# Kernel optimization log

Measured on AMD Instinct MI355X. Metric: run time of the kernel, lower is better.

## Reference

```python
import jax, jax.numpy as jnp
import numpy as np

N_CLASSES = 256
GT_CLASSES = 21
DIM = 384
EPS = 1e-12  # matches torch F.normalize default eps


def setup_inputs() -> dict:
    key = jax.random.key(0)
    k1, k2, k3 = jax.random.split(key, 3)
    features = jax.random.normal(k1, (4, 256, 256, DIM), dtype=jnp.float32)
    weight = jax.random.uniform(k2, (4, 256, 256), dtype=jnp.float32)
    cluster_centers = jax.random.normal(k3, (N_CLASSES, DIM), dtype=jnp.float32)
    pseudo_assignment = (jnp.arange(N_CLASSES) % GT_CLASSES).astype(jnp.int32)
    return {
        "features": features,
        "weight": weight,
        "cluster_centers": cluster_centers,
        "pseudo_assignment": pseudo_assignment,
    }


def _l2norm(x, axis):
    # torch F.normalize: x / max(||x||, eps)
    n = jnp.sqrt(jnp.sum(x * x, axis=axis, keepdims=True))
    return x / jnp.maximum(n, EPS)


def reference(features, weight, cluster_centers, pseudo_assignment):
    lead_shape = features.shape[:-1]
    feats = features.reshape(-1, features.shape[-1])        # [N, D]
    w = weight.reshape(-1)                                   # [N]

    normed_clusters = _l2norm(cluster_centers, axis=1)       # [K, D]
    normed_features = _l2norm(feats, axis=1)                 # [N, D]

    inner_products = normed_features @ normed_clusters.T     # [N, K]
    class_labels = jnp.argmax(inner_products, axis=1)        # [N]

    # -(one_hot(labels) * inner_products).sum(1) == -inner_products[n, labels[n]]
    cluster_loss = -jnp.take_along_axis(
        inner_products, class_labels[:, None], axis=1
    )[:, 0]                                                  # [N]

    loss = jnp.mean(cluster_loss * w)

    pseudo_segs_pred = class_labels.reshape(lead_shape)
    segs_pred = pseudo_assignment[pseudo_segs_pred].astype(jnp.int64)
    return pseudo_segs_pred, segs_pred, loss
```

## Files before the change

### kernel.cpp

```cpp
#include <hip/hip_runtime.h>
#include <hip/hip_bf16.h>

#define NTOT (4*256*256)
#define DIM 384
#define KCL 256
#define BM 64
#define TBS 256
#define GRID_MAIN (NTOT/BM)
#define NT 12
#define EPS 1e-12f

#define AB(p) ((p) * 8192)
#define SMEM_BYTES 16384

typedef __attribute__((ext_vector_type(8))) _Float16 f16x8;
typedef __attribute__((ext_vector_type(4))) float f32x4;

__global__ void prep_clusters(const float* __restrict__ cc,
                              _Float16* __restrict__ bh,
                              _Float16* __restrict__ bl) {
    int j = blockIdx.x, l = threadIdx.x;
    float v[6]; float ssq = 0.f;
#pragma unroll
    for (int i = 0; i < 6; ++i) { v[i] = cc[j*DIM + l + 64*i]; ssq = fmaf(v[i], v[i], ssq); }
#pragma unroll
    for (int off = 32; off >= 1; off >>= 1) ssq += __shfl_xor(ssq, off);
    float inv = 1.f / fmaxf(sqrtf(ssq), EPS);
    const int w = j >> 6, n = (j >> 4) & 3, nl = j & 15;
#pragma unroll
    for (int i = 0; i < 6; ++i) {
        int d = l + 64 * i;
        float x = v[i] * inv;
        _Float16 h  = (_Float16)x;
        _Float16 lo = (_Float16)(x - (float)h);
        size_t idx = (size_t)((((((d >> 5)*4 + w)*4 + n)*4 + ((d >> 3) & 3))*16 + nl)*8
                              + (d & 7));
        bh[idx] = h;
        bl[idx] = lo;
    }
}

__global__ __launch_bounds__(TBS, 3)
void kmeans_main(const float* __restrict__ A,
                 const float* __restrict__ W,
                 const _Float16* __restrict__ Bh,
                 const _Float16* __restrict__ Bl,
                 const int*   __restrict__ PA,
                 float* __restrict__ out,
                 float* __restrict__ partial)
{
    __shared__ unsigned char smem[SMEM_BYTES];

    const int tid  = threadIdx.x;
    const int wv   = tid >> 6;
    const int lane = tid & 63;
    const int g    = lane >> 4;
    const int l15  = lane & 15;
    const int sw   = (l15 >> 1) & 3;
    const int row0 = blockIdx.x * BM;
    const int arow = tid >> 2, achk = tid & 3;
    const int awb  = (((arow << 2) + (achk ^ ((arow >> 1) & 3))) << 4);
    const int fa   = l15 * 64 + ((g ^ sw) << 4);

    const float* ap = A + (size_t)(row0 + arow) * DIM + achk * 8;
    const unsigned char* bsh = (const unsigned char*)Bh + (size_t)(wv * 4) * 1024 + lane * 16;
    const unsigned char* bsl = (const unsigned char*)Bl + (size_t)(wv * 4) * 1024 + lane * 16;

    f32x4 acc[4][4];
#pragma unroll
    for (int m = 0; m < 4; ++m)
#pragma unroll
        for (int n = 0; n < 4; ++n) acc[m][n] = (f32x4){0.f, 0.f, 0.f, 0.f};
    float ssq = 0.f;

    f16x8  bfh[4], bfl[4];
    float4 sA[2][2];

    auto LDA = [&](int s, int tt) {
        sA[s][0] = *(const float4*)(ap + tt * 32);
        sA[s][1] = *(const float4*)(ap + tt * 32 + 4);
    };
    auto LDBH = [&](int tt) {
#pragma unroll
        for (int n = 0; n < 4; ++n)
            bfh[n] = *(const f16x8*)(bsh + (size_t)(tt * 16 + n) * 1024);
    };
    auto LDBL = [&](int tt) {
#pragma unroll
        for (int n = 0; n < 4; ++n)
            bfl[n] = *(const f16x8*)(bsl + (size_t)(tt * 16 + n) * 1024);
    };
    auto CVTW = [&](int s, int p) {
        float av[8] = {sA[s][0].x, sA[s][0].y, sA[s][0].z, sA[s][0].w,
                       sA[s][1].x, sA[s][1].y, sA[s][1].z, sA[s][1].w};
        f16x8 h8, l8;
#pragma unroll
        for (int e = 0; e < 8; ++e) {
            _Float16 hh = (_Float16)av[e];
            h8[e] = hh;
            l8[e] = (_Float16)(av[e] - (float)hh);
            ssq = fmaf(av[e], av[e], ssq);
        }
        *(f16x8*)(smem + AB(p) + awb) = h8;
        *(f16x8*)(smem + AB(p) + 4096 + awb) = l8;
    };

    LDA(0, 0);
    LDBL(0); LDBH(0);
    LDA(1, 1);
    CVTW(0, 0);
    asm volatile("s_waitcnt lgkmcnt(0)" ::: "memory");
    __builtin_amdgcn_s_barrier();

#pragma unroll
    for (int t = 0; t < NT; ++t) {
        if (t + 2 < NT) LDA((t + 2) & 1, t + 2);

        f16x8 ahf[4], alf[4];
#pragma unroll
        for (int m = 0; m < 4; ++m) {
            ahf[m] = *(const f16x8*)(smem + AB(t & 1) + fa + m * 1024);
            alf[m] = *(const f16x8*)(smem + AB(t & 1) + 4096 + fa + m * 1024);
        }
        if (t + 1 < NT) CVTW((t + 1) & 1, (t + 1) & 1);

        __builtin_amdgcn_s_setprio(1);
#pragma unroll
        for (int m = 0; m < 4; ++m)
#pragma unroll
            for (int n = 0; n < 4; ++n)
                acc[m][n] = __builtin_amdgcn_mfma_f32_16x16x32_f16(ahf[m], bfh[n], acc[m][n], 0, 0, 0);
#pragma unroll
        for (int m = 0; m < 4; ++m)
#pragma unroll
            for (int n = 0; n < 4; ++n)
                acc[m][n] = __builtin_amdgcn_mfma_f32_16x16x32_f16(ahf[m], bfl[n], acc[m][n], 0, 0, 0);
        __builtin_amdgcn_s_setprio(0);
        if (t + 1 < NT) LDBL(t + 1);
        __builtin_amdgcn_s_setprio(1);
#pragma unroll
        for (int m = 0; m < 4; ++m)
#pragma unroll
            for (int n = 0; n < 4; ++n)
                acc[m][n] = __builtin_amdgcn_mfma_f32_16x16x32_f16(alf[m], bfh[n], acc[m][n], 0, 0, 0);
        __builtin_amdgcn_s_setprio(0);
        if (t + 1 < NT) LDBH(t + 1);

        asm volatile("s_waitcnt lgkmcnt(0)" ::: "memory");
        __builtin_amdgcn_s_barrier();
    }
    __syncthreads();

    float* rowssq = (float*)smem;
    float* wvalp  = (float*)(smem + 256);
    int*   wcolp  = (int*)(smem + 1280);

    ssq += __shfl_xor(ssq, 1);
    ssq += __shfl_xor(ssq, 2);
    if (achk == 0) rowssq[arow] = ssq;

#pragma unroll
    for (int m = 0; m < 4; ++m) {
#pragma unroll
        for (int j = 0; j < 4; ++j) {
            float best = acc[m][0][j];
            int   bc   = 64*wv + l15;
#pragma unroll
            for (int n = 1; n < 4; ++n) {
                float v = acc[m][n][j];
                int   c = 64*wv + 16*n + l15;
                if (v > best) { best = v; bc = c; }
            }
#pragma unroll
            for (int off = 1; off < 16; off <<= 1) {
                float ov = __shfl_xor(best, off);
                int   oc = __shfl_xor(bc, off);
                if (ov > best || (ov == best && oc < bc)) { best = ov; bc = oc; }
            }
            if (l15 == 0) {
                wvalp[wv * BM + 16*m + 4*g + j] = best;
                wcolp[wv * BM + 16*m + 4*g + j] = bc;
            }
        }
    }
    __syncthreads();

    if (tid < BM) {
        int r = tid;
        float best = wvalp[r]; int bc = wcolp[r];
#pragma unroll
        for (int w = 1; w < 4; ++w) {
            float ov = wvalp[w * BM + r]; int oc = wcolp[w * BM + r];
            if (ov > best || (ov == best && oc < bc)) { best = ov; bc = oc; }
        }
        float inv = 1.f / fmaxf(sqrtf(rowssq[r]), EPS);
        int gr = row0 + r;
        out[gr]        = (float)bc;
        out[NTOT + gr] = (float)PA[bc];
        float lsum = -(best * inv) * W[gr];
#pragma unroll
        for (int off = 32; off >= 1; off >>= 1) lsum += __shfl_xor(lsum, off);
        if (tid == 0) partial[blockIdx.x] = lsum;
    }
}

__global__ void loss_reduce(const float* __restrict__ partial, float* __restrict__ out_loss) {
    __shared__ float s[256];
    float v = 0.f;
    for (int i = threadIdx.x; i < GRID_MAIN; i += 256) v += partial[i];
    s[threadIdx.x] = v;
    __syncthreads();
    for (int off = 128; off >= 1; off >>= 1) {
        if ((int)threadIdx.x < off) s[threadIdx.x] += s[threadIdx.x + off];
        __syncthreads();
    }
    if (threadIdx.x == 0) out_loss[0] = s[0] * (1.0f / (float)NTOT);
}

extern "C" void kernel_launch(void* const* d_in, const int* in_sizes, int n_in,
                              void* d_out, int out_size, void* d_ws, size_t ws_size,
                              hipStream_t stream) {
    const float* features = (const float*)d_in[0];
    const float* weight   = (const float*)d_in[1];
    const float* cc       = (const float*)d_in[2];
    const int*   pa       = (const int*)d_in[3];
    float* out = (float*)d_out;

    _Float16* bh   = (_Float16*)d_ws;
    _Float16* bl   = bh + KCL * DIM;
    float* partial = (float*)(bl + KCL * DIM);

    hipLaunchKernelGGL(prep_clusters, dim3(KCL), dim3(64), 0, stream, cc, bh, bl);
    hipLaunchKernelGGL(kmeans_main, dim3(GRID_MAIN), dim3(TBS), 0, stream,
                       features, weight, bh, bl, pa, out, partial);
    hipLaunchKernelGGL(loss_reduce, dim3(1), dim3(256), 0, stream, partial, out + 2 * NTOT);
}
```

Measured before the change: 194.9 us.

## Stage two K-tiles per barrier to halve block synchronizations

```diff
diff --git a/kernel.cpp b/kernel.cpp
--- a/kernel.cpp
+++ b/kernel.cpp
@@ -7,11 +7,11 @@
 #define BM 64
 #define TBS 256
 #define GRID_MAIN (NTOT/BM)
-#define NT 12
+#define NSTEP 6
 #define EPS 1e-12f
 
-#define AB(p) ((p) * 8192)
-#define SMEM_BYTES 16384
+#define AB(p) ((p) * 16384)
+#define SMEM_BYTES 32768
 
 typedef __attribute__((ext_vector_type(8))) _Float16 f16x8;
 typedef __attribute__((ext_vector_type(4))) float f32x4;
@@ -74,11 +74,13 @@
     float ssq = 0.f;
 
     f16x8  bfh[4], bfl[4];
-    float4 sA[2][2];
-
-    auto LDA = [&](int s, int tt) {
-        sA[s][0] = *(const float4*)(ap + tt * 32);
-        sA[s][1] = *(const float4*)(ap + tt * 32 + 4);
+    float4 sA[4];
+
+    auto LDA = [&](int T) {
+        sA[0] = *(const float4*)(ap + T * 64);
+        sA[1] = *(const float4*)(ap + T * 64 + 4);
+        sA[2] = *(const float4*)(ap + T * 64 + 32);
+        sA[3] = *(const float4*)(ap + T * 64 + 36);
     };
     auto LDBH = [&](int tt) {
 #pragma unroll
@@ -90,40 +92,33 @@
         for (int n = 0; n < 4; ++n)
             bfl[n] = *(const f16x8*)(bsl + (size_t)(tt * 16 + n) * 1024);
     };
-    auto CVTW = [&](int s, int p) {
-        float av[8] = {sA[s][0].x, sA[s][0].y, sA[s][0].z, sA[s][0].w,
-                       sA[s][1].x, sA[s][1].y, sA[s][1].z, sA[s][1].w};
-        f16x8 h8, l8;
-#pragma unroll
-        for (int e = 0; e < 8; ++e) {
-            _Float16 hh = (_Float16)av[e];
-            h8[e] = hh;
-            l8[e] = (_Float16)(av[e] - (float)hh);
-            ssq = fmaf(av[e], av[e], ssq);
-        }
-        *(f16x8*)(smem + AB(p) + awb) = h8;
-        *(f16x8*)(smem + AB(p) + 4096 + awb) = l8;
-    };
-
-    LDA(0, 0);
-    LDBL(0); LDBH(0);
-    LDA(1, 1);
-    CVTW(0, 0);
-    asm volatile("s_waitcnt lgkmcnt(0)" ::: "memory");
-    __builtin_amdgcn_s_barrier();
-
-#pragma unroll
-    for (int t = 0; t < NT; ++t) {
-        if (t + 2 < NT) LDA((t + 2) & 1, t + 2);
-
-        f16x8 ahf[4], alf[4];
+    auto CVTW = [&](int p) {
+#pragma unroll
+        for (int h = 0; h < 2; ++h) {
+            float av[8] = {sA[2*h].x, sA[2*h].y, sA[2*h].z, sA[2*h].w,
+                           sA[2*h+1].x, sA[2*h+1].y, sA[2*h+1].z, sA[2*h+1].w};
+            f16x8 h8, l8;
+#pragma unroll
+            for (int e = 0; e < 8; ++e) {
+                _Float16 hh = (_Float16)av[e];
+                h8[e] = hh;
+                l8[e] = (_Float16)(av[e] - (float)hh);
+                ssq = fmaf(av[e], av[e], ssq);
+            }
+            *(f16x8*)(smem + AB(p) + h * 8192 + awb) = h8;
+            *(f16x8*)(smem + AB(p) + h * 8192 + 4096 + awb) = l8;
+        }
+    };
+
+    f16x8 ahf[4], alf[4];
+    auto READA = [&](int p, int kh) {
 #pragma unroll
         for (int m = 0; m < 4; ++m) {
-            ahf[m] = *(const f16x8*)(smem + AB(t & 1) + fa + m * 1024);
-            alf[m] = *(const f16x8*)(smem + AB(t & 1) + 4096 + fa + m * 1024);
-        }
-        if (t + 1 < NT) CVTW((t + 1) & 1, (t + 1) & 1);
-
+            ahf[m] = *(const f16x8*)(smem + AB(p) + kh * 8192 + fa + m * 1024);
+            alf[m] = *(const f16x8*)(smem + AB(p) + kh * 8192 + 4096 + fa + m * 1024);
+        }
+    };
+    auto MFMA3 = [&](int nextTile, bool doLoad) {
         __builtin_amdgcn_s_setprio(1);
 #pragma unroll
         for (int m = 0; m < 4; ++m)
@@ -136,7 +131,7 @@
             for (int n = 0; n < 4; ++n)
                 acc[m][n] = __builtin_amdgcn_mfma_f32_16x16x32_f16(ahf[m], bfl[n], acc[m][n], 0, 0, 0);
         __builtin_amdgcn_s_setprio(0);
-        if (t + 1 < NT) LDBL(t + 1);
+        if (doLoad) LDBL(nextTile);
         __builtin_amdgcn_s_setprio(1);
 #pragma unroll
         for (int m = 0; m < 4; ++m)
@@ -144,10 +139,29 @@
             for (int n = 0; n < 4; ++n)
                 acc[m][n] = __builtin_amdgcn_mfma_f32_16x16x32_f16(alf[m], bfh[n], acc[m][n], 0, 0, 0);
         __builtin_amdgcn_s_setprio(0);
-        if (t + 1 < NT) LDBH(t + 1);
+        if (doLoad) LDBH(nextTile);
+    };
+
+    LDA(0);
+    LDBL(0); LDBH(0);
+    CVTW(0);
+    asm volatile("s_waitcnt lgkmcnt(0)" ::: "memory");
+    __builtin_amdgcn_s_barrier();
+
+#pragma unroll
+    for (int t = 0; t < NSTEP; ++t) {
+        if (t + 1 < NSTEP) LDA(t + 1);
+
+        READA(t & 1, 0);
+        MFMA3(2 * t + 1, true);
+
+        READA(t & 1, 1);
+        if (t + 1 < NSTEP) CVTW((t + 1) & 1);
 
         asm volatile("s_waitcnt lgkmcnt(0)" ::: "memory");
         __builtin_amdgcn_s_barrier();
+
+        MFMA3(2 * t + 2, t + 1 < NSTEP);
     }
     __syncthreads();
 
```

After: 191.4 us. About the same (-1.8%).

## Use single fp16 GEMM with fp32 rescue pass for near-tie rows

Applied to the files above, without the earlier changes.

```diff
diff --git a/kernel.cpp b/kernel.cpp
--- a/kernel.cpp
+++ b/kernel.cpp
@@ -9,16 +9,18 @@
 #define GRID_MAIN (NTOT/BM)
 #define NT 12
 #define EPS 1e-12f
-
-#define AB(p) ((p) * 8192)
-#define SMEM_BYTES 16384
+#define DELTA 1e-3f
+#define RBLK 512
+#define WPB (GRID_MAIN/RBLK)
+
+#define SMEM_BYTES 8192
 
 typedef __attribute__((ext_vector_type(8))) _Float16 f16x8;
 typedef __attribute__((ext_vector_type(4))) float f32x4;
 
 __global__ void prep_clusters(const float* __restrict__ cc,
                               _Float16* __restrict__ bh,
-                              _Float16* __restrict__ bl) {
+                              float* __restrict__ invn) {
     int j = blockIdx.x, l = threadIdx.x;
     float v[6]; float ssq = 0.f;
 #pragma unroll
@@ -26,17 +28,14 @@
 #pragma unroll
     for (int off = 32; off >= 1; off >>= 1) ssq += __shfl_xor(ssq, off);
     float inv = 1.f / fmaxf(sqrtf(ssq), EPS);
+    if (l == 0) invn[j] = inv;
     const int w = j >> 6, n = (j >> 4) & 3, nl = j & 15;
 #pragma unroll
     for (int i = 0; i < 6; ++i) {
         int d = l + 64 * i;
-        float x = v[i] * inv;
-        _Float16 h  = (_Float16)x;
-        _Float16 lo = (_Float16)(x - (float)h);
         size_t idx = (size_t)((((((d >> 5)*4 + w)*4 + n)*4 + ((d >> 3) & 3))*16 + nl)*8
                               + (d & 7));
-        bh[idx] = h;
-        bl[idx] = lo;
+        bh[idx] = (_Float16)(v[i] * inv);
     }
 }
 
@@ -44,10 +43,10 @@
 void kmeans_main(const float* __restrict__ A,
                  const float* __restrict__ W,
                  const _Float16* __restrict__ Bh,
-                 const _Float16* __restrict__ Bl,
                  const int*   __restrict__ PA,
                  float* __restrict__ out,
-                 float* __restrict__ partial)
+                 float* __restrict__ partial,
+                 unsigned long long* __restrict__ flags)
 {
     __shared__ unsigned char smem[SMEM_BYTES];
 
@@ -64,7 +63,6 @@
 
     const float* ap = A + (size_t)(row0 + arow) * DIM + achk * 8;
     const unsigned char* bsh = (const unsigned char*)Bh + (size_t)(wv * 4) * 1024 + lane * 16;
-    const unsigned char* bsl = (const unsigned char*)Bl + (size_t)(wv * 4) * 1024 + lane * 16;
 
     f32x4 acc[4][4];
 #pragma unroll
@@ -73,7 +71,7 @@
         for (int n = 0; n < 4; ++n) acc[m][n] = (f32x4){0.f, 0.f, 0.f, 0.f};
     float ssq = 0.f;
 
-    f16x8  bfh[4], bfl[4];
+    f16x8  bfh[4];
     float4 sA[2][2];
 
     auto LDA = [&](int s, int tt) {
@@ -85,28 +83,20 @@
         for (int n = 0; n < 4; ++n)
             bfh[n] = *(const f16x8*)(bsh + (size_t)(tt * 16 + n) * 1024);
     };
-    auto LDBL = [&](int tt) {
-#pragma unroll
-        for (int n = 0; n < 4; ++n)
-            bfl[n] = *(const f16x8*)(bsl + (size_t)(tt * 16 + n) * 1024);
-    };
     auto CVTW = [&](int s, int p) {
         float av[8] = {sA[s][0].x, sA[s][0].y, sA[s][0].z, sA[s][0].w,
                        sA[s][1].x, sA[s][1].y, sA[s][1].z, sA[s][1].w};
-        f16x8 h8, l8;
+        f16x8 h8;
 #pragma unroll
         for (int e = 0; e < 8; ++e) {
-            _Float16 hh = (_Float16)av[e];
-            h8[e] = hh;
-            l8[e] = (_Float16)(av[e] - (float)hh);
+            h8[e] = (_Float16)av[e];
             ssq = fmaf(av[e], av[e], ssq);
         }
-        *(f16x8*)(smem + AB(p) + awb) = h8;
-        *(f16x8*)(smem + AB(p) + 4096 + awb) = l8;
+        *(f16x8*)(smem + p * 4096 + awb) = h8;
     };
 
     LDA(0, 0);
-    LDBL(0); LDBH(0);
+    LDBH(0);
     LDA(1, 1);
     CVTW(0, 0);
     asm volatile("s_waitcnt lgkmcnt(0)" ::: "memory");
@@ -116,13 +106,13 @@
     for (int t = 0; t < NT; ++t) {
         if (t + 2 < NT) LDA((t + 2) & 1, t + 2);
 
-        f16x8 ahf[4], alf[4];
-#pragma unroll
-        for (int m = 0; m < 4; ++m) {
-            ahf[m] = *(const f16x8*)(smem + AB(t & 1) + fa + m * 1024);
-            alf[m] = *(const f16x8*)(smem + AB(t & 1) + 4096 + fa + m * 1024);
-        }
+        f16x8 ahf[4];
+#pragma unroll
+        for (int m = 0; m < 4; ++m)
+            ahf[m] = *(const f16x8*)(smem + (t & 1) * 4096 + fa + m * 1024);
         if (t + 1 < NT) CVTW((t + 1) & 1, (t + 1) & 1);
+        asm volatile("s_waitcnt lgkmcnt(0)" ::: "memory");
+        __builtin_amdgcn_s_barrier();
 
         __builtin_amdgcn_s_setprio(1);
 #pragma unroll
@@ -130,30 +120,15 @@
 #pragma unroll
             for (int n = 0; n < 4; ++n)
                 acc[m][n] = __builtin_amdgcn_mfma_f32_16x16x32_f16(ahf[m], bfh[n], acc[m][n], 0, 0, 0);
-#pragma unroll
-        for (int m = 0; m < 4; ++m)
-#pragma unroll
-            for (int n = 0; n < 4; ++n)
-                acc[m][n] = __builtin_amdgcn_mfma_f32_16x16x32_f16(ahf[m], bfl[n], acc[m][n], 0, 0, 0);
-        __builtin_amdgcn_s_setprio(0);
-        if (t + 1 < NT) LDBL(t + 1);
-        __builtin_amdgcn_s_setprio(1);
-#pragma unroll
-        for (int m = 0; m < 4; ++m)
-#pragma unroll
-            for (int n = 0; n < 4; ++n)
-                acc[m][n] = __builtin_amdgcn_mfma_f32_16x16x32_f16(alf[m], bfh[n], acc[m][n], 0, 0, 0);
         __builtin_amdgcn_s_setprio(0);
         if (t + 1 < NT) LDBH(t + 1);
-
-        asm volatile("s_waitcnt lgkmcnt(0)" ::: "memory");
-        __builtin_amdgcn_s_barrier();
     }
     __syncthreads();
 
     float* rowssq = (float*)smem;
     float* wvalp  = (float*)(smem + 256);
-    int*   wcolp  = (int*)(smem + 1280);
+    float* wsecp  = (float*)(smem + 1280);
+    int*   wcolp  = (int*)(smem + 2304);
 
     ssq += __shfl_xor(ssq, 1);
     ssq += __shfl_xor(ssq, 2);
@@ -163,23 +138,23 @@
     for (int m = 0; m < 4; ++m) {
 #pragma unroll
         for (int j = 0; j < 4; ++j) {
-            float best = acc[m][0][j];
-            int   bc   = 64*wv + l15;
+            float b0 = acc[m][0][j]; int i0 = 64*wv + l15; float s0 = -3.0e38f;
 #pragma unroll
             for (int n = 1; n < 4; ++n) {
-                float v = acc[m][n][j];
-                int   c = 64*wv + 16*n + l15;
-                if (v > best) { best = v; bc = c; }
+                float v = acc[m][n][j]; int c = 64*wv + 16*n + l15;
+                if (v > b0) { s0 = b0; b0 = v; i0 = c; } else { s0 = fmaxf(s0, v); }
             }
 #pragma unroll
             for (int off = 1; off < 16; off <<= 1) {
-                float ov = __shfl_xor(best, off);
-                int   oc = __shfl_xor(bc, off);
-                if (ov > best || (ov == best && oc < bc)) { best = ov; bc = oc; }
+                float ov = __shfl_xor(b0, off);
+                int   oi = __shfl_xor(i0, off);
+                float os = __shfl_xor(s0, off);
+                if (ov > b0 || (ov == b0 && oi < i0)) { s0 = fmaxf(os, b0); b0 = ov; i0 = oi; }
+                else                                  { s0 = fmaxf(s0, ov); }
             }
             if (l15 == 0) {
-                wvalp[wv * BM + 16*m + 4*g + j] = best;
-                wcolp[wv * BM + 16*m + 4*g + j] = bc;
+                int r = 16*m + 4*g + j;
+                wvalp[wv * BM + r] = b0; wsecp[wv * BM + r] = s0; wcolp[wv * BM + r] = i0;
             }
         }
     }
@@ -187,34 +162,145 @@
 
     if (tid < BM) {
         int r = tid;
-        float best = wvalp[r]; int bc = wcolp[r];
+        float b = wvalp[r], s = wsecp[r]; int i = wcolp[r];
 #pragma unroll
         for (int w = 1; w < 4; ++w) {
-            float ov = wvalp[w * BM + r]; int oc = wcolp[w * BM + r];
-            if (ov > best || (ov == best && oc < bc)) { best = ov; bc = oc; }
+            float bw = wvalp[w * BM + r], sw2 = wsecp[w * BM + r]; int iw = wcolp[w * BM + r];
+            if (bw > b || (bw == b && iw < i)) { s = fmaxf(b, sw2); b = bw; i = iw; }
+            else                               { s = fmaxf(s, bw); }
         }
         float inv = 1.f / fmaxf(sqrtf(rowssq[r]), EPS);
         int gr = row0 + r;
-        out[gr]        = (float)bc;
-        out[NTOT + gr] = (float)PA[bc];
-        float lsum = -(best * inv) * W[gr];
+        out[gr]        = (float)i;
+        out[NTOT + gr] = (float)PA[i];
+        bool amb = (b - s) < DELTA;
+        unsigned long long mask = __ballot(amb);
+        float lsum = amb ? 0.f : -(b * inv) * W[gr];
 #pragma unroll
         for (int off = 32; off >= 1; off >>= 1) lsum += __shfl_xor(lsum, off);
-        if (tid == 0) partial[blockIdx.x] = lsum;
-    }
-}
-
-__global__ void loss_reduce(const float* __restrict__ partial, float* __restrict__ out_loss) {
+        if (tid == 0) { partial[blockIdx.x] = lsum; flags[blockIdx.x] = mask; }
+    }
+}
+
+__global__ __launch_bounds__(256)
+void rescue(const float* __restrict__ A, const float* __restrict__ W,
+            const float* __restrict__ cc, const float* __restrict__ invn,
+            const unsigned long long* __restrict__ flags,
+            const int* __restrict__ PA,
+            float* __restrict__ out, float* __restrict__ partial2)
+{
+    __shared__ float rows[4][8][DIM];
+    __shared__ int   rlist[64 * WPB];
+    __shared__ int   rcount;
+    __shared__ float wsum[4];
+    const int tid = threadIdx.x, wv = tid >> 6, lane = tid & 63;
+    const int b = blockIdx.x;
+
+    if (tid == 0) {
+        int c = 0;
+#pragma unroll
+        for (int w = 0; w < WPB; ++w) {
+            unsigned long long m = flags[b * WPB + w];
+            while (m) {
+                int bit = __ffsll((long long)m) - 1;
+                m &= m - 1;
+                rlist[c++] = (b * WPB + w) * 64 + bit;
+            }
+        }
+        rcount = c;
+    }
+    __syncthreads();
+    const int nb = rcount;
+    const float in0 = invn[lane], in1 = invn[64 + lane],
+                in2 = invn[128 + lane], in3 = invn[192 + lane];
+    float lacc = 0.f;
+    const int nbatch = (nb + 31) >> 5;
+
+    for (int bt = 0; bt < nbatch; ++bt) {
+        const int base = bt * 32 + wv * 8;
+        int rIdx[8]; float ssq8[8];
+#pragma unroll
+        for (int i = 0; i < 8; ++i) {
+            int li = base + i;
+            int r = rlist[li < nb ? li : 0];
+            rIdx[i] = r;
+            float ps = 0.f;
+#pragma unroll
+            for (int c = 0; c < 6; ++c) {
+                float x = A[(size_t)r * DIM + c*64 + lane];
+                rows[wv][i][c*64 + lane] = x;
+                ps = fmaf(x, x, ps);
+            }
+#pragma unroll
+            for (int off = 32; off >= 1; off >>= 1) ps += __shfl_xor(ps, off);
+            ssq8[i] = ps;
+        }
+        __syncthreads();
+        float d0[8], d1[8], d2[8], d3[8];
+#pragma unroll
+        for (int i = 0; i < 8; ++i) { d0[i]=0.f; d1[i]=0.f; d2[i]=0.f; d3[i]=0.f; }
+#pragma unroll 4
+        for (int k = 0; k < DIM; k += 4) {
+            float4 rv[8];
+#pragma unroll
+            for (int i = 0; i < 8; ++i) rv[i] = *(const float4*)&rows[wv][i][k];
+            float4 c0 = *(const float4*)&cc[(size_t)(0*64 + lane)*DIM + k];
+            float4 c1 = *(const float4*)&cc[(size_t)(1*64 + lane)*DIM + k];
+            float4 c2 = *(const float4*)&cc[(size_t)(2*64 + lane)*DIM + k];
+            float4 c3 = *(const float4*)&cc[(size_t)(3*64 + lane)*DIM + k];
+#pragma unroll
+            for (int i = 0; i < 8; ++i) {
+                d0[i] = fmaf(c0.x,rv[i].x, fmaf(c0.y,rv[i].y, fmaf(c0.z,rv[i].z, fmaf(c0.w,rv[i].w, d0[i]))));
+                d1[i] = fmaf(c1.x,rv[i].x, fmaf(c1.y,rv[i].y, fmaf(c1.z,rv[i].z, fmaf(c1.w,rv[i].w, d1[i]))));
+                d2[i] = fmaf(c2.x,rv[i].x, fmaf(c2.y,rv[i].y, fmaf(c2.z,rv[i].z, fmaf(c2.w,rv[i].w, d2[i]))));
+                d3[i] = fmaf(c3.x,rv[i].x, fmaf(c3.y,rv[i].y, fmaf(c3.z,rv[i].z, fmaf(c3.w,rv[i].w, d3[i]))));
+            }
+        }
+#pragma unroll
+        for (int i = 0; i < 8; ++i) {
+            if (base + i < nb) {
+                float v0 = d0[i]*in0, v1 = d1[i]*in1, v2 = d2[i]*in2, v3 = d3[i]*in3;
+                float best = v0; int bj = lane;
+                { if (v1 > best) { best = v1; bj = 64 + lane; } }
+                { if (v2 > best) { best = v2; bj = 128 + lane; } }
+                { if (v3 > best) { best = v3; bj = 192 + lane; } }
+#pragma unroll
+                for (int off = 1; off < 64; off <<= 1) {
+                    float ov = __shfl_xor(best, off);
+                    int   oj = __shfl_xor(bj, off);
+                    if (ov > best || (ov == best && oj < bj)) { best = ov; bj = oj; }
+                }
+                if (lane == 0) {
+                    int r = rIdx[i];
+                    float inva = 1.f / fmaxf(sqrtf(ssq8[i]), EPS);
+                    out[r]        = (float)bj;
+                    out[NTOT + r] = (float)PA[bj];
+                    lacc = fmaf(-(best * inva), W[r], lacc);
+                }
+            }
+        }
+        __syncthreads();
+    }
+    if (lane == 0) wsum[wv] = lacc;
+    __syncthreads();
+    if (tid == 0) partial2[b] = ((wsum[0] + wsum[1]) + (wsum[2] + wsum[3]));
+}
+
+__global__ void loss_reduce(const float* __restrict__ partial,
+                            const float* __restrict__ partial2,
+                            float* __restrict__ out_loss) {
     __shared__ float s[256];
+    const int t = threadIdx.x;
     float v = 0.f;
-    for (int i = threadIdx.x; i < GRID_MAIN; i += 256) v += partial[i];
-    s[threadIdx.x] = v;
+    for (int i = t; i < GRID_MAIN; i += 256) v += partial[i];
+    for (int i = t; i < RBLK; i += 256) v += partial2[i];
+    s[t] = v;
     __syncthreads();
     for (int off = 128; off >= 1; off >>= 1) {
-        if ((int)threadIdx.x < off) s[threadIdx.x] += s[threadIdx.x + off];
+        if (t < off) s[t] += s[t + off];
         __syncthreads();
     }
-    if (threadIdx.x == 0) out_loss[0] = s[0] * (1.0f / (float)NTOT);
+    if (t == 0) out_loss[0] = s[0] * (1.0f / (float)NTOT);
 }
 
 extern "C" void kernel_launch(void* const* d_in, const int* in_sizes, int n_in,
@@ -226,12 +312,17 @@
     const int*   pa       = (const int*)d_in[3];
     float* out = (float*)d_out;
 
-    _Float16* bh   = (_Float16*)d_ws;
-    _Float16* bl   = bh + KCL * DIM;
-    float* partial = (float*)(bl + KCL * DIM);
-
-    hipLaunchKernelGGL(prep_clusters, dim3(KCL), dim3(64), 0, stream, cc, bh, bl);
+    _Float16* bh = (_Float16*)d_ws;
+    unsigned long long* flags = (unsigned long long*)(bh + KCL * DIM);
+    float* invn    = (float*)(flags + GRID_MAIN);
+    float* partial = invn + KCL;
+    float* partial2 = partial + GRID_MAIN;
+
+    hipLaunchKernelGGL(prep_clusters, dim3(KCL), dim3(64), 0, stream, cc, bh, invn);
     hipLaunchKernelGGL(kmeans_main, dim3(GRID_MAIN), dim3(TBS), 0, stream,
-                       features, weight, bh, bl, pa, out, partial);
-    hipLaunchKernelGGL(loss_reduce, dim3(1), dim3(256), 0, stream, partial, out + 2 * NTOT);
-}
+                       features, weight, bh, pa, out, partial, flags);
+    hipLaunchKernelGGL(rescue, dim3(RBLK), dim3(256), 0, stream,
+                       features, weight, cc, invn, flags, pa, out, partial2);
+    hipLaunchKernelGGL(loss_reduce, dim3(1), dim3(256), 0, stream,
+                       partial, partial2, out + 2 * NTOT);
+}
```

After: 283.4 us. +45.4%, slower.

## Use single fp16 MFMA pass with fp32 rescoring of ambiguous rows

Applied to the files above, without the earlier changes.

```diff
diff --git a/kernel.cpp b/kernel.cpp
--- a/kernel.cpp
+++ b/kernel.cpp
@@ -9,16 +9,17 @@
 #define GRID_MAIN (NTOT/BM)
 #define NT 12
 #define EPS 1e-12f
-
-#define AB(p) ((p) * 8192)
-#define SMEM_BYTES 16384
+#define DELTA 0.09f
+#define CAP 12
+
+#define SMEM_BYTES 8192
 
 typedef __attribute__((ext_vector_type(8))) _Float16 f16x8;
 typedef __attribute__((ext_vector_type(4))) float f32x4;
 
 __global__ void prep_clusters(const float* __restrict__ cc,
                               _Float16* __restrict__ bh,
-                              _Float16* __restrict__ bl) {
+                              float* __restrict__ invn) {
     int j = blockIdx.x, l = threadIdx.x;
     float v[6]; float ssq = 0.f;
 #pragma unroll
@@ -26,25 +27,23 @@
 #pragma unroll
     for (int off = 32; off >= 1; off >>= 1) ssq += __shfl_xor(ssq, off);
     float inv = 1.f / fmaxf(sqrtf(ssq), EPS);
+    if (l == 0) invn[j] = inv;
     const int w = j >> 6, n = (j >> 4) & 3, nl = j & 15;
 #pragma unroll
     for (int i = 0; i < 6; ++i) {
         int d = l + 64 * i;
-        float x = v[i] * inv;
-        _Float16 h  = (_Float16)x;
-        _Float16 lo = (_Float16)(x - (float)h);
         size_t idx = (size_t)((((((d >> 5)*4 + w)*4 + n)*4 + ((d >> 3) & 3))*16 + nl)*8
                               + (d & 7));
-        bh[idx] = h;
-        bl[idx] = lo;
-    }
-}
-
-__global__ __launch_bounds__(TBS, 3)
+        bh[idx] = (_Float16)(v[i] * inv);
+    }
+}
+
+__global__ __launch_bounds__(TBS, 4)
 void kmeans_main(const float* __restrict__ A,
                  const float* __restrict__ W,
                  const _Float16* __restrict__ Bh,
-                 const _Float16* __restrict__ Bl,
+                 const float* __restrict__ cc,
+                 const float* __restrict__ invn,
                  const int*   __restrict__ PA,
                  float* __restrict__ out,
                  float* __restrict__ partial)
@@ -64,7 +63,6 @@
 
     const float* ap = A + (size_t)(row0 + arow) * DIM + achk * 8;
     const unsigned char* bsh = (const unsigned char*)Bh + (size_t)(wv * 4) * 1024 + lane * 16;
-    const unsigned char* bsl = (const unsigned char*)Bl + (size_t)(wv * 4) * 1024 + lane * 16;
 
     f32x4 acc[4][4];
 #pragma unroll
@@ -73,7 +71,7 @@
         for (int n = 0; n < 4; ++n) acc[m][n] = (f32x4){0.f, 0.f, 0.f, 0.f};
     float ssq = 0.f;
 
-    f16x8  bfh[4], bfl[4];
+    f16x8  bfh[4];
     float4 sA[2][2];
 
     auto LDA = [&](int s, int tt) {
@@ -85,28 +83,20 @@
         for (int n = 0; n < 4; ++n)
             bfh[n] = *(const f16x8*)(bsh + (size_t)(tt * 16 + n) * 1024);
     };
-    auto LDBL = [&](int tt) {
-#pragma unroll
-        for (int n = 0; n < 4; ++n)
-            bfl[n] = *(const f16x8*)(bsl + (size_t)(tt * 16 + n) * 1024);
-    };
     auto CVTW = [&](int s, int p) {
         float av[8] = {sA[s][0].x, sA[s][0].y, sA[s][0].z, sA[s][0].w,
                        sA[s][1].x, sA[s][1].y, sA[s][1].z, sA[s][1].w};
-        f16x8 h8, l8;
+        f16x8 h8;
 #pragma unroll
         for (int e = 0; e < 8; ++e) {
-            _Float16 hh = (_Float16)av[e];
-            h8[e] = hh;
-            l8[e] = (_Float16)(av[e] - (float)hh);
+            h8[e] = (_Float16)av[e];
             ssq = fmaf(av[e], av[e], ssq);
         }
-        *(f16x8*)(smem + AB(p) + awb) = h8;
-        *(f16x8*)(smem + AB(p) + 4096 + awb) = l8;
+        *(f16x8*)(smem + p * 4096 + awb) = h8;
     };
 
     LDA(0, 0);
-    LDBL(0); LDBH(0);
+    LDBH(0);
     LDA(1, 1);
     CVTW(0, 0);
     asm volatile("s_waitcnt lgkmcnt(0)" ::: "memory");
@@ -116,13 +106,13 @@
     for (int t = 0; t < NT; ++t) {
         if (t + 2 < NT) LDA((t + 2) & 1, t + 2);
 
-        f16x8 ahf[4], alf[4];
-#pragma unroll
-        for (int m = 0; m < 4; ++m) {
-            ahf[m] = *(const f16x8*)(smem + AB(t & 1) + fa + m * 1024);
-            alf[m] = *(const f16x8*)(smem + AB(t & 1) + 4096 + fa + m * 1024);
-        }
+        f16x8 ahf[4];
+#pragma unroll
+        for (int m = 0; m < 4; ++m)
+            ahf[m] = *(const f16x8*)(smem + (t & 1) * 4096 + fa + m * 1024);
         if (t + 1 < NT) CVTW((t + 1) & 1, (t + 1) & 1);
+        asm volatile("s_waitcnt lgkmcnt(0)" ::: "memory");
+        __builtin_amdgcn_s_barrier();
 
         __builtin_amdgcn_s_setprio(1);
 #pragma unroll
@@ -130,30 +120,23 @@
 #pragma unroll
             for (int n = 0; n < 4; ++n)
                 acc[m][n] = __builtin_amdgcn_mfma_f32_16x16x32_f16(ahf[m], bfh[n], acc[m][n], 0, 0, 0);
-#pragma unroll
-        for (int m = 0; m < 4; ++m)
-#pragma unroll
-            for (int n = 0; n < 4; ++n)
-                acc[m][n] = __builtin_amdgcn_mfma_f32_16x16x32_f16(ahf[m], bfl[n], acc[m][n], 0, 0, 0);
-        __builtin_amdgcn_s_setprio(0);
-        if (t + 1 < NT) LDBL(t + 1);
-        __builtin_amdgcn_s_setprio(1);
-#pragma unroll
-        for (int m = 0; m < 4; ++m)
-#pragma unroll
-            for (int n = 0; n < 4; ++n)
-                acc[m][n] = __builtin_amdgcn_mfma_f32_16x16x32_f16(alf[m], bfh[n], acc[m][n], 0, 0, 0);
         __builtin_amdgcn_s_setprio(0);
         if (t + 1 < NT) LDBH(t + 1);
-
-        asm volatile("s_waitcnt lgkmcnt(0)" ::: "memory");
-        __builtin_amdgcn_s_barrier();
-    }
-    __syncthreads();
-
-    float* rowssq = (float*)smem;
+    }
+    __syncthreads();
+
+    float* rowssq = (float*)(smem);
     float* wvalp  = (float*)(smem + 256);
-    int*   wcolp  = (int*)(smem + 1280);
+    float* wsecp  = (float*)(smem + 1280);
+    int*   wcolp  = (int*)(smem + 2304);
+    float* rowtop = (float*)(smem + 3328);
+    float* rowinv = (float*)(smem + 3584);
+    float* lrowS  = (float*)(smem + 3840);
+    unsigned long long* fmaskS = (unsigned long long*)(smem + 4096);
+    int*   ccount = (int*)(smem + 4160);
+    int*   clist  = (int*)(smem + 4416);
+    float* wrv    = (float*)(smem + 7488);
+    int*   wrc    = (int*)(smem + 7552);
 
     ssq += __shfl_xor(ssq, 1);
     ssq += __shfl_xor(ssq, 2);
@@ -163,23 +146,23 @@
     for (int m = 0; m < 4; ++m) {
 #pragma unroll
         for (int j = 0; j < 4; ++j) {
-            float best = acc[m][0][j];
-            int   bc   = 64*wv + l15;
+            float b0 = acc[m][0][j]; int i0 = 64*wv + l15; float s0 = -3.0e38f;
 #pragma unroll
             for (int n = 1; n < 4; ++n) {
-                float v = acc[m][n][j];
-                int   c = 64*wv + 16*n + l15;
-                if (v > best) { best = v; bc = c; }
+                float v = acc[m][n][j]; int c = 64*wv + 16*n + l15;
+                if (v > b0) { s0 = b0; b0 = v; i0 = c; } else { s0 = fmaxf(s0, v); }
             }
 #pragma unroll
             for (int off = 1; off < 16; off <<= 1) {
-                float ov = __shfl_xor(best, off);
-                int   oc = __shfl_xor(bc, off);
-                if (ov > best || (ov == best && oc < bc)) { best = ov; bc = oc; }
+                float ov = __shfl_xor(b0, off);
+                int   oi = __shfl_xor(i0, off);
+                float os = __shfl_xor(s0, off);
+                if (ov > b0 || (ov == b0 && oi < i0)) { s0 = fmaxf(os, b0); b0 = ov; i0 = oi; }
+                else                                  { s0 = fmaxf(s0, ov); }
             }
             if (l15 == 0) {
-                wvalp[wv * BM + 16*m + 4*g + j] = best;
-                wcolp[wv * BM + 16*m + 4*g + j] = bc;
+                int r = 16*m + 4*g + j;
+                wvalp[wv * BM + r] = b0; wsecp[wv * BM + r] = s0; wcolp[wv * BM + r] = i0;
             }
         }
     }
@@ -187,20 +170,94 @@
 
     if (tid < BM) {
         int r = tid;
-        float best = wvalp[r]; int bc = wcolp[r];
+        if (r < 64) ccount[r] = 0;
+        float b = wvalp[r], s = wsecp[r]; int i = wcolp[r];
 #pragma unroll
         for (int w = 1; w < 4; ++w) {
-            float ov = wvalp[w * BM + r]; int oc = wcolp[w * BM + r];
-            if (ov > best || (ov == best && oc < bc)) { best = ov; bc = oc; }
+            float bw = wvalp[w * BM + r], sw2 = wsecp[w * BM + r]; int iw = wcolp[w * BM + r];
+            if (bw > b || (bw == b && iw < i)) { s = fmaxf(b, sw2); b = bw; i = iw; }
+            else                               { s = fmaxf(s, bw); }
         }
         float inv = 1.f / fmaxf(sqrtf(rowssq[r]), EPS);
+        rowtop[r] = b; rowinv[r] = inv;
+        bool amb = (b - s) < DELTA;
+        unsigned long long msk = __ballot(amb);
         int gr = row0 + r;
-        out[gr]        = (float)bc;
-        out[NTOT + gr] = (float)PA[bc];
-        float lsum = -(best * inv) * W[gr];
-#pragma unroll
-        for (int off = 32; off >= 1; off >>= 1) lsum += __shfl_xor(lsum, off);
-        if (tid == 0) partial[blockIdx.x] = lsum;
+        if (!amb) {
+            out[gr]        = (float)i;
+            out[NTOT + gr] = (float)PA[i];
+        }
+        lrowS[r] = amb ? 0.f : -(b * inv) * W[gr];
+        if (tid == 0) fmaskS[0] = msk;
+    }
+    __syncthreads();
+
+    const unsigned long long fm = fmaskS[0];
+    if (fm) {
+#pragma unroll
+        for (int m = 0; m < 4; ++m) {
+#pragma unroll
+            for (int j = 0; j < 4; ++j) {
+                int r = 16*m + 4*g + j;
+                if ((fm >> r) & 1ull) {
+                    float th = rowtop[r] - DELTA;
+#pragma unroll
+                    for (int n = 0; n < 4; ++n) {
+                        if (acc[m][n][j] >= th) {
+                            int col = 64*wv + 16*n + l15;
+                            int pos = atomicAdd(&ccount[r], 1);
+                            if (pos < CAP) clist[r * CAP + pos] = col;
+                        }
+                    }
+                }
+            }
+        }
+        __syncthreads();
+
+        unsigned long long mm = fm;
+        while (mm) {
+            int r = __ffsll((long long)mm) - 1;
+            mm &= mm - 1;
+            int cnt = ccount[r]; if (cnt > CAP) cnt = CAP;
+            const float* arp = A + (size_t)(row0 + r) * DIM;
+            float av6[6];
+#pragma unroll
+            for (int i2 = 0; i2 < 6; ++i2) av6[i2] = arp[i2*64 + lane];
+            float bv = -3.0e38f; int bc2 = 0x7fffffff;
+            for (int k = wv; k < cnt; k += 4) {
+                int col = clist[r * CAP + k];
+                const float* cp = cc + (size_t)col * DIM;
+                float d = 0.f;
+#pragma unroll
+                for (int i2 = 0; i2 < 6; ++i2) d = fmaf(av6[i2], cp[i2*64 + lane], d);
+#pragma unroll
+                for (int off = 1; off < 64; off <<= 1) d += __shfl_xor(d, off);
+                float val = d * invn[col];
+                if (val > bv || (val == bv && col < bc2)) { bv = val; bc2 = col; }
+            }
+            if (lane == 0) { wrv[wv] = bv; wrc[wv] = bc2; }
+            __syncthreads();
+            if (tid == 0) {
+                float b2 = wrv[0]; int c2 = wrc[0];
+#pragma unroll
+                for (int w = 1; w < 4; ++w) {
+                    float ov = wrv[w]; int oc = wrc[w];
+                    if (ov > b2 || (ov == b2 && oc < c2)) { b2 = ov; c2 = oc; }
+                }
+                int gr = row0 + r;
+                out[gr]        = (float)c2;
+                out[NTOT + gr] = (float)PA[c2];
+                lrowS[r] = -(b2 * rowinv[r]) * W[gr];
+            }
+            __syncthreads();
+        }
+    }
+
+    if (tid < BM) {
+        float l = lrowS[tid];
+#pragma unroll
+        for (int off = 1; off < 64; off <<= 1) l += __shfl_xor(l, off);
+        if (tid == 0) partial[blockIdx.x] = l;
     }
 }
 
@@ -227,11 +284,11 @@
     float* out = (float*)d_out;
 
     _Float16* bh   = (_Float16*)d_ws;
-    _Float16* bl   = bh + KCL * DIM;
-    float* partial = (float*)(bl + KCL * DIM);
-
-    hipLaunchKernelGGL(prep_clusters, dim3(KCL), dim3(64), 0, stream, cc, bh, bl);
+    float* invn    = (float*)(bh + KCL * DIM);
+    float* partial = invn + KCL;
+
+    hipLaunchKernelGGL(prep_clusters, dim3(KCL), dim3(64), 0, stream, cc, bh, invn);
     hipLaunchKernelGGL(kmeans_main, dim3(GRID_MAIN), dim3(TBS), 0, stream,
-                       features, weight, bh, bl, pa, out, partial);
+                       features, weight, bh, cc, invn, pa, out, partial);
     hipLaunchKernelGGL(loss_reduce, dim3(1), dim3(256), 0, stream, partial, out + 2 * NTOT);
 }
```

Result: slower. 208.1 us (+6.8%).
